# Optimization experiments

Measured on AMD Instinct MI355X. Metric: run time of the kernel, lower is better.

## Reference

```python
import jax, jax.numpy as jnp
import numpy as np

B = 128
N_ATOMS = 4096
NB, NA, NT = 4095, 4094, 4093
MAX_LEN = 5 * NT  # 20465, longest packed column (torsions)
EPS = 1e-8


def setup_inputs() -> dict:
    key = jax.random.key(0)
    ks = jax.random.split(key, 24)
    feats = jnp.zeros((B, MAX_LEN, 9), jnp.float32)
    # col 0: atom type ids
    atoms = jax.random.randint(ks[0], (B, N_ATOMS), 0, 6)
    # col 5: coords, flattened (N_ATOMS, 3)
    coords = jax.random.normal(ks[1], (B, N_ATOMS, 3), jnp.float32) * 5.0
    # col 6: bonds (i, j, type)
    bonds = jnp.stack([
        jax.random.randint(ks[2], (B, NB), 0, N_ATOMS),
        jax.random.randint(ks[3], (B, NB), 0, N_ATOMS),
        jax.random.randint(ks[4], (B, NB), 0, 15)], axis=-1)
    # col 7: angles (i, j, k, type)
    angles = jnp.stack([
        jax.random.randint(ks[5], (B, NA), 0, N_ATOMS),
        jax.random.randint(ks[6], (B, NA), 0, N_ATOMS),
        jax.random.randint(ks[7], (B, NA), 0, N_ATOMS),
        jax.random.randint(ks[8], (B, NA), 0, 13)], axis=-1)
    # col 8: torsions (i, j, k, l, type)
    tors = jnp.stack([
        jax.random.randint(ks[9], (B, NT), 0, N_ATOMS),
        jax.random.randint(ks[10], (B, NT), 0, N_ATOMS),
        jax.random.randint(ks[11], (B, NT), 0, N_ATOMS),
        jax.random.randint(ks[12], (B, NT), 0, N_ATOMS),
        jax.random.randint(ks[13], (B, NT), 0, 25)], axis=-1)
    feats = feats.at[:, :N_ATOMS, 0].set(atoms.astype(jnp.float32))
    feats = feats.at[:, :3 * N_ATOMS, 5].set(coords.reshape(B, -1))
    feats = feats.at[:, :3 * NB, 6].set(bonds.reshape(B, -1).astype(jnp.float32))
    feats = feats.at[:, :4 * NA, 7].set(angles.reshape(B, -1).astype(jnp.float32))
    feats = feats.at[:, :5 * NT, 8].set(tors.reshape(B, -1).astype(jnp.float32))
    lengths = jnp.tile(jnp.array(
        [[N_ATOMS, 0, 0, 0, 0, 3 * N_ATOMS, 3 * NB, 4 * NA, 5 * NT]],
        jnp.int32), (B, 1))
    bond_type = jnp.stack([jnp.ones(15), jax.random.uniform(ks[14], (15,), minval=1.0, maxval=2.0)], -1).astype(jnp.float32)
    angle_type = jnp.stack([jnp.ones(13), jax.random.uniform(ks[15], (13,), minval=1.0, maxval=3.0)], -1).astype(jnp.float32)
    tor_type = jnp.stack([jnp.ones(25), jax.random.uniform(ks[16], (25,), minval=0.0, maxval=3.14)], -1).astype(jnp.float32)
    multiplicity = jax.random.randint(ks[17], (25,), 1, 4)
    opt_pars = jax.random.uniform(ks[18], (47,), minval=0.5, maxval=1.5).astype(jnp.float32)
    return {"features": feats, "lengths": lengths, "bond_type": bond_type,
            "angle_type": angle_type, "tor_type": tor_type,
            "multiplicity": multiplicity, "opt_pars": opt_pars}


def _sample_energy(f, bond_type, angle_type, tor_type, multiplicity, opt_pars):
    coords = f[:3 * N_ATOMS, 5].reshape(-1, 3)                      # [N,3]
    bonds = f[:3 * NB, 6].astype(jnp.int32).reshape(-1, 3)          # [NB,3]
    angles = f[:4 * NA, 7].astype(jnp.int32).reshape(-1, 4)         # [NA,4]
    tors = f[:5 * NT, 8].astype(jnp.int32).reshape(-1, 5)           # [NT,5]

    # bonds: harmonic k*(r - r0)^2
    d = coords[bonds[:, 0]] - coords[bonds[:, 1]]
    r = jnp.sqrt(jnp.sum(d * d, -1) + EPS)
    pb = bond_type[bonds[:, 2]]
    e_bond = opt_pars[0] * jnp.sum(pb[:, 0] * (r - pb[:, 1]) ** 2)

    # angles: harmonic k*(theta - theta0)^2
    v1 = coords[angles[:, 0]] - coords[angles[:, 1]]
    v2 = coords[angles[:, 2]] - coords[angles[:, 1]]
    cosang = jnp.sum(v1 * v2, -1) / (
        jnp.sqrt(jnp.sum(v1 * v1, -1) + EPS) * jnp.sqrt(jnp.sum(v2 * v2, -1) + EPS))
    theta = jnp.arccos(jnp.clip(cosang, -1.0 + 1e-6, 1.0 - 1e-6))
    pa = angle_type[angles[:, 3]]
    e_ang = opt_pars[1] * jnp.sum(pa[:, 0] * (theta - pa[:, 1]) ** 2)

    # torsions: periodic k*(1 + cos(n*phi - delta))
    ci, cj, ck, cl = (coords[tors[:, m]] for m in range(4))
    b1, b2, b3 = cj - ci, ck - cj, cl - ck
    n1 = jnp.cross(b1, b2)
    n2 = jnp.cross(b2, b3)
    b2n = b2 / jnp.sqrt(jnp.sum(b2 * b2, -1, keepdims=True) + EPS)
    m1 = jnp.cross(n1, b2n)
    phi = jnp.arctan2(jnp.sum(m1 * n2, -1), jnp.sum(n1 * n2, -1))
    pt = tor_type[tors[:, 4]]
    n_mult = multiplicity[tors[:, 4]].astype(jnp.float32)
    e_tor = opt_pars[2] * jnp.sum(pt[:, 0] * (1.0 + jnp.cos(n_mult * phi - pt[:, 1])))

    return jnp.stack([e_bond, e_ang, e_tor])


def reference(features, lengths, bond_type, angle_type, tor_type, multiplicity, opt_pars):
    # lengths are uniform across batch (constants above); vmap over batch dim
    return jax.vmap(_sample_energy, in_axes=(0, None, None, None, None, None))(
        features, bond_type, angle_type, tor_type, multiplicity, opt_pars)
```

## Files before the change

kernel.cpp:

```cpp
#include <hip/hip_runtime.h>
#include <math.h>

#define BATCH   128
#define N_ATOMS 4096
#define NB      4095
#define NA      4094
#define NT      4093
#define MAX_LEN (5 * NT)
#define FSTRIDE ((size_t)MAX_LEN * 9)
#define EPSV    1e-8f
#define PARTS   4
#define THREADS 256

__global__ __launch_bounds__(THREADS) void
local_energy_kernel(const float* __restrict__ F,
                    const float* __restrict__ bond_type,
                    const float* __restrict__ angle_type,
                    const float* __restrict__ tor_type,
                    const int*   __restrict__ multiplicity,
                    const float* __restrict__ opt_pars,
                    float*       __restrict__ out)
{
    __shared__ float scx[N_ATOMS];
    __shared__ float scy[N_ATOMS];
    __shared__ float scz[N_ATOMS];
    __shared__ float sbt[30];
    __shared__ float sat[26];
    __shared__ float stt[50];
    __shared__ float smu[25];
    __shared__ float sred[PARTS == 4 ? 12 : 12];

    const int blk = blockIdx.x;
    const int s   = blk >> 2;
    const int p   = blk & 3;
    const int tid = threadIdx.x;
    const float* __restrict__ Fb = F + (size_t)s * FSTRIDE;

    if (tid < 30)                      sbt[tid]       = bond_type[tid];
    else if (tid >= 32 && tid < 58)    sat[tid - 32]  = angle_type[tid - 32];
    else if (tid >= 64 && tid < 114)   stt[tid - 64]  = tor_type[tid - 64];
    else if (tid >= 128 && tid < 153)  smu[tid - 128] = (float)multiplicity[tid - 128];

    for (int l = tid; l < 3 * N_ATOMS; l += THREADS) {
        float v = Fb[(size_t)l * 9 + 5];
        int a = l / 3;
        int c = l - 3 * a;
        if (c == 0)      scx[a] = v;
        else if (c == 1) scy[a] = v;
        else             scz[a] = v;
    }
    __syncthreads();

    float e_bond = 0.0f, e_ang = 0.0f, e_tor = 0.0f;

    {
        const int chunk = (NB + PARTS - 1) / PARTS;
        const int lo = p * chunk;
        const int hi = (lo + chunk < NB) ? (lo + chunk) : NB;
        for (int i = lo + tid; i < hi; i += THREADS) {
            const float* bp = Fb + (size_t)(3 * i) * 9 + 6;
            int a0 = (int)bp[0];
            int a1 = (int)bp[9];
            int bt = (int)bp[18];
            float dx = scx[a0] - scx[a1];
            float dy = scy[a0] - scy[a1];
            float dz = scz[a0] - scz[a1];
            float r  = sqrtf(dx*dx + dy*dy + dz*dz + EPSV);
            float k0 = sbt[bt * 2 + 0];
            float r0 = sbt[bt * 2 + 1];
            float t  = r - r0;
            e_bond += k0 * t * t;
        }
    }

    {
        const int chunk = (NA + PARTS - 1) / PARTS;
        const int lo = p * chunk;
        const int hi = (lo + chunk < NA) ? (lo + chunk) : NA;
        for (int i = lo + tid; i < hi; i += THREADS) {
            const float* ap = Fb + (size_t)(4 * i) * 9 + 7;
            int a0 = (int)ap[0];
            int a1 = (int)ap[9];
            int a2 = (int)ap[18];
            int at = (int)ap[27];
            float v1x = scx[a0] - scx[a1];
            float v1y = scy[a0] - scy[a1];
            float v1z = scz[a0] - scz[a1];
            float v2x = scx[a2] - scx[a1];
            float v2y = scy[a2] - scy[a1];
            float v2z = scz[a2] - scz[a1];
            float d12 = v1x*v2x + v1y*v2y + v1z*v2z;
            float n1  = sqrtf(v1x*v1x + v1y*v1y + v1z*v1z + EPSV);
            float n2  = sqrtf(v2x*v2x + v2y*v2y + v2z*v2z + EPSV);
            float cosang = d12 / (n1 * n2);
            cosang = fminf(fmaxf(cosang, -1.0f + 1e-6f), 1.0f - 1e-6f);
            float theta = acosf(cosang);
            float k0 = sat[at * 2 + 0];
            float t0 = sat[at * 2 + 1];
            float t  = theta - t0;
            e_ang += k0 * t * t;
        }
    }

    {
        const int chunk = (NT + PARTS - 1) / PARTS;
        const int lo = p * chunk;
        const int hi = (lo + chunk < NT) ? (lo + chunk) : NT;
        for (int i = lo + tid; i < hi; i += THREADS) {
            const float* tp = Fb + (size_t)(5 * i) * 9 + 8;
            int ai = (int)tp[0];
            int aj = (int)tp[9];
            int ak = (int)tp[18];
            int al = (int)tp[27];
            int tt = (int)tp[36];

            float cix = scx[ai], ciy = scy[ai], ciz = scz[ai];
            float cjx = scx[aj], cjy = scy[aj], cjz = scz[aj];
            float ckx = scx[ak], cky = scy[ak], ckz = scz[ak];
            float clx = scx[al], cly = scy[al], clz = scz[al];

            float b1x = cjx - cix, b1y = cjy - ciy, b1z = cjz - ciz;
            float b2x = ckx - cjx, b2y = cky - cjy, b2z = ckz - cjz;
            float b3x = clx - ckx, b3y = cly - cky, b3z = clz - ckz;

            float n1x = b1y*b2z - b1z*b2y;
            float n1y = b1z*b2x - b1x*b2z;
            float n1z = b1x*b2y - b1y*b2x;
            float n2x = b2y*b3z - b2z*b3y;
            float n2y = b2z*b3x - b2x*b3z;
            float n2z = b2x*b3y - b2y*b3x;

            float b2len = sqrtf(b2x*b2x + b2y*b2y + b2z*b2z + EPSV);
            float inv   = 1.0f / b2len;
            float bnx = b2x * inv, bny = b2y * inv, bnz = b2z * inv;

            float m1x = n1y*bnz - n1z*bny;
            float m1y = n1z*bnx - n1x*bnz;
            float m1z = n1x*bny - n1y*bnx;

            float sy = m1x*n2x + m1y*n2y + m1z*n2z;
            float sx = n1x*n2x + n1y*n2y + n1z*n2z;
            float phi = atan2f(sy, sx);

            float k0  = stt[tt * 2 + 0];
            float ph0 = stt[tt * 2 + 1];
            float nm  = smu[tt];
            e_tor += k0 * (1.0f + cosf(nm * phi - ph0));
        }
    }

    for (int off = 32; off > 0; off >>= 1) {
        e_bond += __shfl_down(e_bond, off);
        e_ang  += __shfl_down(e_ang,  off);
        e_tor  += __shfl_down(e_tor,  off);
    }
    const int wave = tid >> 6;
    const int lane = tid & 63;
    if (lane == 0) {
        sred[wave * 3 + 0] = e_bond;
        sred[wave * 3 + 1] = e_ang;
        sred[wave * 3 + 2] = e_tor;
    }
    __syncthreads();
    if (tid == 0) {
        float eb = 0.0f, ea = 0.0f, et = 0.0f;
        for (int w = 0; w < THREADS / 64; ++w) {
            eb += sred[w * 3 + 0];
            ea += sred[w * 3 + 1];
            et += sred[w * 3 + 2];
        }
        atomicAdd(&out[s * 3 + 0], opt_pars[0] * eb);
        atomicAdd(&out[s * 3 + 1], opt_pars[1] * ea);
        atomicAdd(&out[s * 3 + 2], opt_pars[2] * et);
    }
}

extern "C" void kernel_launch(void* const* d_in, const int* in_sizes, int n_in,
                              void* d_out, int out_size, void* d_ws, size_t ws_size,
                              hipStream_t stream) {
    const float* F            = (const float*)d_in[0];
    const float* bond_type    = (const float*)d_in[2];
    const float* angle_type   = (const float*)d_in[3];
    const float* tor_type     = (const float*)d_in[4];
    const int*   multiplicity = (const int*)  d_in[5];
    const float* opt_pars     = (const float*)d_in[6];
    float* out = (float*)d_out;

    hipMemsetAsync(out, 0, (size_t)out_size * sizeof(float), stream);

    dim3 grid(BATCH * PARTS);
    dim3 block(THREADS);
    local_energy_kernel<<<grid, block, 0, stream>>>(
        F, bond_type, angle_type, tor_type, multiplicity, opt_pars, out);
}
```

Measured before the change: 179.5 us.

## Split each sample across six blocks with XCD-aware mapping and per-atom coord loads

Raises the number of blocks per sample from four to six and remaps block IDs so that consecutive blocks, which are dispatched round-robin over the eight chiplets, cover different samples while the parts of one sample sit in the same chiplet group. This is meant to improve L2 reuse of each sample's feature rows. The coordinate staging loop now handles one atom per thread, dropping the divide and branch, and index arithmetic uses 32-bit offsets. The cost is that each sample's coordinates are staged into shared memory six times instead of four.

```diff
diff --git a/kernel.cpp b/kernel.cpp
--- a/kernel.cpp
+++ b/kernel.cpp
@@ -9,7 +9,7 @@
 #define MAX_LEN (5 * NT)
 #define FSTRIDE ((size_t)MAX_LEN * 9)
 #define EPSV    1e-8f
-#define PARTS   4
+#define PARTS   6
 #define THREADS 256
 
 __global__ __launch_bounds__(THREADS) void
@@ -28,11 +28,13 @@
     __shared__ float sat[26];
     __shared__ float stt[50];
     __shared__ float smu[25];
-    __shared__ float sred[PARTS == 4 ? 12 : 12];
+    __shared__ float sred[12];
 
-    const int blk = blockIdx.x;
-    const int s   = blk >> 2;
-    const int p   = blk & 3;
+    const int b   = blockIdx.x;
+    const int x   = b & 7;
+    const int g   = b >> 3;
+    const int s   = (g & 15) * 8 + x;
+    const int p   = g >> 4;
     const int tid = threadIdx.x;
     const float* __restrict__ Fb = F + (size_t)s * FSTRIDE;
 
@@ -41,13 +43,14 @@
     else if (tid >= 64 && tid < 114)   stt[tid - 64]  = tor_type[tid - 64];
     else if (tid >= 128 && tid < 153)  smu[tid - 128] = (float)multiplicity[tid - 128];
 
-    for (int l = tid; l < 3 * N_ATOMS; l += THREADS) {
-        float v = Fb[(size_t)l * 9 + 5];
-        int a = l / 3;
-        int c = l - 3 * a;
-        if (c == 0)      scx[a] = v;
-        else if (c == 1) scy[a] = v;
-        else             scz[a] = v;
+    for (int a = tid; a < N_ATOMS; a += THREADS) {
+        const float* cp = Fb + 27 * a;
+        float vx = cp[5];
+        float vy = cp[14];
+        float vz = cp[23];
+        scx[a] = vx;
+        scy[a] = vy;
+        scz[a] = vz;
     }
     __syncthreads();
 
@@ -58,7 +61,7 @@
         const int lo = p * chunk;
         const int hi = (lo + chunk < NB) ? (lo + chunk) : NB;
         for (int i = lo + tid; i < hi; i += THREADS) {
-            const float* bp = Fb + (size_t)(3 * i) * 9 + 6;
+            const float* bp = Fb + 27 * i + 6;
             int a0 = (int)bp[0];
             int a1 = (int)bp[9];
             int bt = (int)bp[18];
@@ -78,7 +81,7 @@
         const int lo = p * chunk;
         const int hi = (lo + chunk < NA) ? (lo + chunk) : NA;
         for (int i = lo + tid; i < hi; i += THREADS) {
-            const float* ap = Fb + (size_t)(4 * i) * 9 + 7;
+            const float* ap = Fb + 36 * i + 7;
             int a0 = (int)ap[0];
             int a1 = (int)ap[9];
             int a2 = (int)ap[18];
@@ -107,7 +110,7 @@
         const int lo = p * chunk;
         const int hi = (lo + chunk < NT) ? (lo + chunk) : NT;
         for (int i = lo + tid; i < hi; i += THREADS) {
-            const float* tp = Fb + (size_t)(5 * i) * 9 + 8;
+            const float* tp = Fb + 45 * i + 8;
             int ai = (int)tp[0];
             int aj = (int)tp[9];
             int ak = (int)tp[18];
```

Result: faster. 174.0 us (-3.0%).
